# Kernel optimization log

Hardware: AMD Instinct MI355X
Metric: run time of the kernel (lower is better)

## Reference

```python
import jax, jax.numpy as jnp
import numpy as np

B, S, I, H = 32, 4096, 512, 512
NEG_INF = -1e18


def setup_inputs() -> dict:
    key = jax.random.key(0)
    ks = jax.random.split(key, 8)
    query = jax.random.normal(ks[0], (B, I), dtype=jnp.float32)
    kv = jax.random.normal(ks[1], (B, S, I), dtype=jnp.float32)
    mask = jax.random.randint(ks[2], (B, S), 0, 2).astype(jnp.bool_)
    # q_proj: Linear(I, H) with bias
    lim_q = 1.0 / np.sqrt(I)
    Wq = jax.random.uniform(ks[3], (H, I), minval=-lim_q, maxval=lim_q, dtype=jnp.float32)
    bq = jax.random.uniform(ks[4], (H,), minval=-lim_q, maxval=lim_q, dtype=jnp.float32)
    # k_proj: Conv1d(I, H, kernel_size=1) == pointwise linear; weight squeezed to [H, I]
    Wk = jax.random.uniform(ks[5], (H, I), minval=-lim_q, maxval=lim_q, dtype=jnp.float32)
    bk = jax.random.uniform(ks[6], (H,), minval=-lim_q, maxval=lim_q, dtype=jnp.float32)
    # out: Linear(H, 1, bias=False), init uniform(-1, 1); squeeze to [H]
    Wout = jax.random.uniform(ks[7], (H,), minval=-1.0, maxval=1.0, dtype=jnp.float32)
    return {"query": query, "key": kv, "mask": mask,
            "Wq": Wq, "bq": bq, "Wk": Wk, "bk": bk, "Wout": Wout}


def reference(query, key, mask, Wq, bq, Wk, bk, Wout):
    # q: [B, H]
    q = query @ Wq.T + bq
    # k: conv1d kernel-size-1 == per-position linear -> [B, S, H]
    k = jnp.einsum('bsi,hi->bsh', key, Wk) + bk
    # additive attention score: out((q + k)) -> [B, S]
    scores = jnp.einsum('bsh,h->bs', q[:, None, :] + k, Wout)
    attn_weight = jnp.where(mask, jnp.float32(NEG_INF), scores)
    attn_prob = jax.nn.softmax(attn_weight, axis=-1)
    # bmm(k^T-form [B, H, S], prob [B, S, 1]) -> [B, H]
    attn = jnp.einsum('bsh,bs->bh', k, attn_prob)
    return attn, attn_weight
```

## Files before the change

### kernel.cpp

```cpp
#include <hip/hip_runtime.h>
#include <math.h>

constexpr int B = 32, S = 4096, I = 512, H = 512;
constexpr int CH = 128;
constexpr int NCH = S / CH;
constexpr float NEGV = -1e18f;

constexpr size_t WS_WKD   = 0;
constexpr size_t WS_WQD   = 512;
constexpr size_t WS_CC    = 1024;
constexpr size_t WS_WKT   = 2048;
constexpr size_t WS_PARTS = WS_WKT + (size_t)I*H;

__global__ __launch_bounds__(256) void prep_kernel(
    const float* __restrict__ Wq, const float* __restrict__ bq,
    const float* __restrict__ Wk, const float* __restrict__ bk,
    const float* __restrict__ Wout, float* __restrict__ ws) {
  __shared__ float sh[64 * 65];
  int blk = blockIdx.x;
  int t = threadIdx.x, wv = t >> 6, ln = t & 63;

  if (blk < 16) {
    bool isQ = blk >= 8;
    const float* W = isQ ? Wq : Wk;
    float* out = ws + (isQ ? WS_WQD : WS_WKD);
    int j = (blk & 7) * 64;
    float p = 0.f;
    int h0 = wv * 128;
    #pragma unroll 4
    for (int h = h0; h < h0 + 128; ++h)
      p = fmaf(W[(size_t)h * I + j + ln], Wout[h], p);
    sh[wv * 64 + ln] = p;
    __syncthreads();
    if (t < 64) out[j + t] = sh[t] + sh[64 + t] + sh[128 + t] + sh[192 + t];
  } else if (blk == 16) {
    float p = 0.f;
    for (int h = t; h < H; h += 256) p = fmaf(bq[h] + bk[h], Wout[h], p);
    sh[t] = p;
    __syncthreads();
    for (int o = 128; o; o >>= 1) {
      if (t < o) sh[t] += sh[t + o];
      __syncthreads();
    }
    if (t == 0) ws[WS_CC] = sh[0];
  } else {
    int tt = blk - 17;
    int tr = tt >> 3, tc = tt & 7;
    float* wkT = ws + WS_WKT;
    #pragma unroll 4
    for (int k = 0; k < 16; ++k) {
      int r = wv * 16 + k;
      sh[r * 65 + ln] = Wk[(size_t)(tr * 64 + r) * I + tc * 64 + ln];
    }
    __syncthreads();
    #pragma unroll 4
    for (int k = 0; k < 16; ++k) {
      int r2 = wv * 16 + k;
      wkT[(size_t)(tc * 64 + r2) * H + tr * 64 + ln] = sh[ln * 65 + r2];
    }
  }
}

__global__ __launch_bounds__(256, 4) void main_kernel(
    const float* __restrict__ query,
    const float* __restrict__ key, const int* __restrict__ mask,
    float* __restrict__ ws, float* __restrict__ attn_w) {
  const float* wkd = ws + WS_WKD;
  const float* wqd = ws + WS_WQD;
  float* parts = ws + WS_PARTS;

  int b = blockIdx.x, cidx = blockIdx.y;
  int t = threadIdx.x, wv = t >> 6, ln = t & 63;

  float offb;
  {
    const float* qb = query + (size_t)b * I;
    float p = qb[ln] * wqd[ln];
    #pragma unroll
    for (int k = 1; k < 8; ++k)
      p = fmaf(qb[ln + 64 * k], wqd[ln + 64 * k], p);
    #pragma unroll
    for (int o = 32; o; o >>= 1) p += __shfl_xor(p, o, 64);
    offb = p + ws[WS_CC];
  }

  const float* kb = key + ((size_t)b * S + (size_t)cidx * CH) * I;
  const int* mrow = mask + (size_t)b * S + cidx * CH;
  float* awrow = attn_w + (size_t)b * S + cidx * CH;

  float4 wA = *(const float4*)(wkd + ln * 4);
  float4 wB = *(const float4*)(wkd + 256 + ln * 4);

  float m = -INFINITY, l = 0.f;
  float4 cA = {0.f, 0.f, 0.f, 0.f}, cB = {0.f, 0.f, 0.f, 0.f};

  constexpr int NIT = CH / 8;
  const float* lanep = kb + (size_t)(wv * 2) * I + ln * 4;
  constexpr int ROWSTEP = 8 * I;

  float4 uA0 = *(const float4*)(lanep);
  float4 uB0 = *(const float4*)(lanep + 256);
  float4 uA1 = *(const float4*)(lanep + 512);
  float4 uB1 = *(const float4*)(lanep + 768);
  float4 vA0 = *(const float4*)(lanep + ROWSTEP);
  float4 vB0 = *(const float4*)(lanep + ROWSTEP + 256);
  float4 vA1 = *(const float4*)(lanep + ROWSTEP + 512);
  float4 vB1 = *(const float4*)(lanep + ROWSTEP + 768);

  #pragma unroll 2
  for (int it = 0; it < NIT; ++it) {
    int s = wv * 2 + it * 8;
    int itn = (it + 2 < NIT) ? it + 2 : it;
    const float* kn = lanep + (size_t)itn * ROWSTEP;
    float4 nA0 = *(const float4*)(kn);
    float4 nB0 = *(const float4*)(kn + 256);
    float4 nA1 = *(const float4*)(kn + 512);
    float4 nB1 = *(const float4*)(kn + 768);

    float d0 = uA0.x * wA.x, d1 = uA1.x * wA.x;
    d0 = fmaf(uA0.y, wA.y, d0); d1 = fmaf(uA1.y, wA.y, d1);
    d0 = fmaf(uA0.z, wA.z, d0); d1 = fmaf(uA1.z, wA.z, d1);
    d0 = fmaf(uA0.w, wA.w, d0); d1 = fmaf(uA1.w, wA.w, d1);
    d0 = fmaf(uB0.x, wB.x, d0); d1 = fmaf(uB1.x, wB.x, d1);
    d0 = fmaf(uB0.y, wB.y, d0); d1 = fmaf(uB1.y, wB.y, d1);
    d0 = fmaf(uB0.z, wB.z, d0); d1 = fmaf(uB1.z, wB.z, d1);
    d0 = fmaf(uB0.w, wB.w, d0); d1 = fmaf(uB1.w, wB.w, d1);
    #pragma unroll
    for (int o = 32; o; o >>= 1) {
      d0 += __shfl_xor(d0, o, 64);
      d1 += __shfl_xor(d1, o, 64);
    }

    int2 mm = *(const int2*)(mrow + s);
    float s0 = mm.x ? NEGV : (offb + d0);
    float s1 = mm.y ? NEGV : (offb + d1);
    if (ln == 0) *(float2*)(awrow + s) = float2{s0, s1};

    float mx = fmaxf(s0, s1);
    if (mx > m) {
      float sc = __expf(m - mx);
      l *= sc;
      cA.x *= sc; cA.y *= sc; cA.z *= sc; cA.w *= sc;
      cB.x *= sc; cB.y *= sc; cB.z *= sc; cB.w *= sc;
      m = mx;
    }
    float e0 = __expf(s0 - m);
    float e1 = __expf(s1 - m);
    l += e0 + e1;
    cA.x = fmaf(e0, uA0.x, fmaf(e1, uA1.x, cA.x));
    cA.y = fmaf(e0, uA0.y, fmaf(e1, uA1.y, cA.y));
    cA.z = fmaf(e0, uA0.z, fmaf(e1, uA1.z, cA.z));
    cA.w = fmaf(e0, uA0.w, fmaf(e1, uA1.w, cA.w));
    cB.x = fmaf(e0, uB0.x, fmaf(e1, uB1.x, cB.x));
    cB.y = fmaf(e0, uB0.y, fmaf(e1, uB1.y, cB.y));
    cB.z = fmaf(e0, uB0.z, fmaf(e1, uB1.z, cB.z));
    cB.w = fmaf(e0, uB0.w, fmaf(e1, uB1.w, cB.w));

    uA0 = vA0; uB0 = vB0; uA1 = vA1; uB1 = vB1;
    vA0 = nA0; vB0 = nB0; vA1 = nA1; vB1 = nB1;
  }

  __shared__ float shm[4], shl[4];
  __shared__ float shc[4][512];
  if (ln == 0) { shm[wv] = m; shl[wv] = l; }
  *(float4*)&shc[wv][ln * 4] = cA;
  *(float4*)&shc[wv][256 + ln * 4] = cB;
  __syncthreads();

  float mb = fmaxf(fmaxf(shm[0], shm[1]), fmaxf(shm[2], shm[3]));
  float ew0 = __expf(shm[0] - mb), ew1 = __expf(shm[1] - mb);
  float ew2 = __expf(shm[2] - mb), ew3 = __expf(shm[3] - mb);
  float* slot = parts + ((size_t)b * NCH + cidx) * 514;
  if (t == 0) {
    slot[0] = mb;
    slot[1] = shl[0] * ew0 + shl[1] * ew1 + shl[2] * ew2 + shl[3] * ew3;
  }
  for (int i = t; i < I; i += 256) {
    float acc = shc[0][i] * ew0;
    acc = fmaf(shc[1][i], ew1, acc);
    acc = fmaf(shc[2][i], ew2, acc);
    acc = fmaf(shc[3][i], ew3, acc);
    slot[2 + i] = acc;
  }
}

__global__ __launch_bounds__(256) void finish_kernel(
    const float* __restrict__ bk, float* __restrict__ ws,
    float* __restrict__ attn) {
  const float* parts = ws + WS_PARTS;
  const float* wkT = ws + WS_WKT;
  int b = blockIdx.x, hq = blockIdx.y, t = threadIdx.x;

  __shared__ float eld[NCH], ctx[I], red[256];
  const float* pb = parts + (size_t)b * NCH * 514;

  float m = -INFINITY;
  #pragma unroll 8
  for (int p = 0; p < NCH; ++p) m = fmaxf(m, pb[p * 514]);
  float l = 0.f;
  #pragma unroll 8
  for (int p = 0; p < NCH; ++p) l = fmaf(pb[p * 514 + 1], __expf(pb[p * 514] - m), l);
  float invl = 1.f / l;
  if (t < NCH) eld[t] = __expf(pb[t * 514] - m) * invl;
  __syncthreads();

  {
    float a0 = 0.f, a1 = 0.f;
    #pragma unroll 8
    for (int p = 0; p < NCH; ++p) {
      float e = eld[p];
      a0 = fmaf(pb[p * 514 + 2 + t], e, a0);
      a1 = fmaf(pb[p * 514 + 258 + t], e, a1);
    }
    ctx[t] = a0;
    ctx[t + 256] = a1;
  }
  __syncthreads();

  int h = hq * 128 + (t & 127);
  int ih = t >> 7;
  const float* wc = wkT + (size_t)(ih * 256) * H + h;
  const float* cc = ctx + ih * 256;
  float acc = 0.f;
  #pragma unroll 16
  for (int i = 0; i < 256; ++i) acc = fmaf(cc[i], wc[(size_t)i * H], acc);
  red[t] = acc;
  __syncthreads();
  if (t < 128) attn[(size_t)b * H + h] = red[t] + red[t + 128] + bk[h];
}

extern "C" void kernel_launch(void* const* d_in, const int* in_sizes, int n_in,
                              void* d_out, int out_size, void* d_ws, size_t ws_size,
                              hipStream_t stream) {
  const float* query = (const float*)d_in[0];
  const float* key   = (const float*)d_in[1];
  const int*   mask  = (const int*)d_in[2];
  const float* Wq    = (const float*)d_in[3];
  const float* bq    = (const float*)d_in[4];
  const float* Wk    = (const float*)d_in[5];
  const float* bk    = (const float*)d_in[6];
  const float* Wout  = (const float*)d_in[7];

  float* attn   = (float*)d_out;
  float* attn_w = (float*)d_out + (size_t)B * H;
  float* ws     = (float*)d_ws;

  prep_kernel<<<81, 256, 0, stream>>>(Wq, bq, Wk, bk, Wout, ws);
  main_kernel<<<dim3(B, NCH), 256, 0, stream>>>(query, key, mask, ws, attn_w);
  finish_kernel<<<dim3(B, 4), 256, 0, stream>>>(bk, ws, attn);
}
```

Baseline: 81.71 us.

## Split weight-fold prep, precompute per-batch offset, drop Wk transpose in finish

The prep stage is split into two kernels. prepA spreads the Wout-folding of Wq/Wk over 128 blocks as partial sums, and a single-block prepB reduces those partials and computes each batch's query offset once, instead of every main_kernel block recomputing it. The Wk transpose into workspace is removed; finish_kernel now reads Wk rows directly with float4 loads, one thread per output h. This trades a fourth kernel launch and a serial single-block stage for less prep work and less redundant compute in main_kernel. The finish kernel's per-thread row reads are strided across threads, so the Wk access pattern changes.

```diff
diff --git a/kernel.cpp b/kernel.cpp
--- a/kernel.cpp
+++ b/kernel.cpp
@@ -7,82 +7,94 @@
 constexpr float NEGV = -1e18f;
 
 constexpr size_t WS_WKD   = 0;
-constexpr size_t WS_WQD   = 512;
-constexpr size_t WS_CC    = 1024;
-constexpr size_t WS_WKT   = 2048;
-constexpr size_t WS_PARTS = WS_WKT + (size_t)I*H;
-
-__global__ __launch_bounds__(256) void prep_kernel(
-    const float* __restrict__ Wq, const float* __restrict__ bq,
-    const float* __restrict__ Wk, const float* __restrict__ bk,
+constexpr size_t WS_OFF   = 512;
+constexpr size_t WS_PARTW = 1024;
+constexpr size_t WS_PARTS = 16384;
+
+__global__ __launch_bounds__(256) void prepA_kernel(
+    const float* __restrict__ Wq, const float* __restrict__ Wk,
     const float* __restrict__ Wout, float* __restrict__ ws) {
-  __shared__ float sh[64 * 65];
+  __shared__ float red[4][64];
   int blk = blockIdx.x;
   int t = threadIdx.x, wv = t >> 6, ln = t & 63;
-
-  if (blk < 16) {
-    bool isQ = blk >= 8;
-    const float* W = isQ ? Wq : Wk;
-    float* out = ws + (isQ ? WS_WQD : WS_WKD);
-    int j = (blk & 7) * 64;
-    float p = 0.f;
-    int h0 = wv * 128;
-    #pragma unroll 4
-    for (int h = h0; h < h0 + 128; ++h)
-      p = fmaf(W[(size_t)h * I + j + ln], Wout[h], p);
-    sh[wv * 64 + ln] = p;
+  bool isQ = blk >= 64;
+  const float* W = isQ ? Wq : Wk;
+  int sub = blk & 63;
+  int hs = sub >> 3, jt = sub & 7;
+  int j = jt * 64 + ln;
+
+  float acc = 0.f;
+  int h0 = hs * 64 + wv * 16;
+  #pragma unroll 4
+  for (int r = 0; r < 16; ++r) {
+    int h = h0 + r;
+    acc = fmaf(W[(size_t)h * I + j], Wout[h], acc);
+  }
+  red[wv][ln] = acc;
+  __syncthreads();
+  if (t < 64) {
+    float s = red[0][t] + red[1][t] + red[2][t] + red[3][t];
+    ws[WS_PARTW + (isQ ? 4096 : 0) + hs * 512 + jt * 64 + t] = s;
+  }
+}
+
+__global__ __launch_bounds__(256) void prepB_kernel(
+    const float* __restrict__ query, const float* __restrict__ bq,
+    const float* __restrict__ bk, const float* __restrict__ Wout,
+    float* __restrict__ ws) {
+  __shared__ float wq[512];
+  __shared__ float red2[256];
+  int t = threadIdx.x, wv = t >> 6, ln = t & 63;
+  const float* pk = ws + WS_PARTW;
+
+  #pragma unroll
+  for (int half = 0; half < 2; ++half) {
+    int c = t + half * 256;
+    float sk = 0.f, sq = 0.f;
+    #pragma unroll
+    for (int hs = 0; hs < 8; ++hs) {
+      sk += pk[hs * 512 + c];
+      sq += pk[4096 + hs * 512 + c];
+    }
+    ws[WS_WKD + c] = sk;
+    wq[c] = sq;
+  }
+
+  float p = 0.f;
+  p = fmaf(bq[t] + bk[t], Wout[t], p);
+  p = fmaf(bq[t + 256] + bk[t + 256], Wout[t + 256], p);
+  red2[t] = p;
+  __syncthreads();
+  for (int o = 128; o; o >>= 1) {
+    if (t < o) red2[t] += red2[t + o];
     __syncthreads();
-    if (t < 64) out[j + t] = sh[t] + sh[64 + t] + sh[128 + t] + sh[192 + t];
-  } else if (blk == 16) {
-    float p = 0.f;
-    for (int h = t; h < H; h += 256) p = fmaf(bq[h] + bk[h], Wout[h], p);
-    sh[t] = p;
-    __syncthreads();
-    for (int o = 128; o; o >>= 1) {
-      if (t < o) sh[t] += sh[t + o];
-      __syncthreads();
-    }
-    if (t == 0) ws[WS_CC] = sh[0];
-  } else {
-    int tt = blk - 17;
-    int tr = tt >> 3, tc = tt & 7;
-    float* wkT = ws + WS_WKT;
-    #pragma unroll 4
-    for (int k = 0; k < 16; ++k) {
-      int r = wv * 16 + k;
-      sh[r * 65 + ln] = Wk[(size_t)(tr * 64 + r) * I + tc * 64 + ln];
-    }
-    __syncthreads();
-    #pragma unroll 4
-    for (int k = 0; k < 16; ++k) {
-      int r2 = wv * 16 + k;
-      wkT[(size_t)(tc * 64 + r2) * H + tr * 64 + ln] = sh[ln * 65 + r2];
-    }
+  }
+  float ccv = red2[0];
+  __syncthreads();
+
+  for (int pass = 0; pass < 8; ++pass) {
+    int b = pass * 4 + wv;
+    const float* qb = query + (size_t)b * I;
+    float d = qb[ln] * wq[ln];
+    #pragma unroll
+    for (int k = 1; k < 8; ++k)
+      d = fmaf(qb[ln + 64 * k], wq[ln + 64 * k], d);
+    #pragma unroll
+    for (int o = 32; o; o >>= 1) d += __shfl_xor(d, o, 64);
+    if (ln == 0) ws[WS_OFF + b] = d + ccv;
   }
 }
 
 __global__ __launch_bounds__(256, 4) void main_kernel(
-    const float* __restrict__ query,
     const float* __restrict__ key, const int* __restrict__ mask,
     float* __restrict__ ws, float* __restrict__ attn_w) {
   const float* wkd = ws + WS_WKD;
-  const float* wqd = ws + WS_WQD;
   float* parts = ws + WS_PARTS;
 
   int b = blockIdx.x, cidx = blockIdx.y;
   int t = threadIdx.x, wv = t >> 6, ln = t & 63;
 
-  float offb;
-  {
-    const float* qb = query + (size_t)b * I;
-    float p = qb[ln] * wqd[ln];
-    #pragma unroll
-    for (int k = 1; k < 8; ++k)
-      p = fmaf(qb[ln + 64 * k], wqd[ln + 64 * k], p);
-    #pragma unroll
-    for (int o = 32; o; o >>= 1) p += __shfl_xor(p, o, 64);
-    offb = p + ws[WS_CC];
-  }
+  float offb = ws[WS_OFF + b];
 
   const float* kb = key + ((size_t)b * S + (size_t)cidx * CH) * I;
   const int* mrow = mask + (size_t)b * S + cidx * CH;
@@ -185,13 +197,12 @@
 }
 
 __global__ __launch_bounds__(256) void finish_kernel(
-    const float* __restrict__ bk, float* __restrict__ ws,
-    float* __restrict__ attn) {
+    const float* __restrict__ Wk, const float* __restrict__ bk,
+    float* __restrict__ ws, float* __restrict__ attn) {
   const float* parts = ws + WS_PARTS;
-  const float* wkT = ws + WS_WKT;
   int b = blockIdx.x, hq = blockIdx.y, t = threadIdx.x;
 
-  __shared__ float eld[NCH], ctx[I], red[256];
+  __shared__ float eld[NCH], ctx[I];
   const float* pb = parts + (size_t)b * NCH * 514;
 
   float m = -INFINITY;
@@ -217,16 +228,21 @@
   }
   __syncthreads();
 
-  int h = hq * 128 + (t & 127);
-  int ih = t >> 7;
-  const float* wc = wkT + (size_t)(ih * 256) * H + h;
-  const float* cc = ctx + ih * 256;
-  float acc = 0.f;
-  #pragma unroll 16
-  for (int i = 0; i < 256; ++i) acc = fmaf(cc[i], wc[(size_t)i * H], acc);
-  red[t] = acc;
-  __syncthreads();
-  if (t < 128) attn[(size_t)b * H + h] = red[t] + red[t + 128] + bk[h];
+  int h = hq * 256 + t;
+  const float4* wrow = (const float4*)(Wk + (size_t)h * I);
+  float a0 = 0.f, a1 = 0.f, a2 = 0.f, a3 = 0.f;
+  #pragma unroll 8
+  for (int c = 0; c < 128; c += 4) {
+    float4 w0 = wrow[c],     x0 = *(const float4*)(ctx + c * 4);
+    float4 w1 = wrow[c + 1], x1 = *(const float4*)(ctx + c * 4 + 4);
+    float4 w2 = wrow[c + 2], x2 = *(const float4*)(ctx + c * 4 + 8);
+    float4 w3 = wrow[c + 3], x3 = *(const float4*)(ctx + c * 4 + 12);
+    a0 = fmaf(w0.x, x0.x, fmaf(w0.y, x0.y, fmaf(w0.z, x0.z, fmaf(w0.w, x0.w, a0))));
+    a1 = fmaf(w1.x, x1.x, fmaf(w1.y, x1.y, fmaf(w1.z, x1.z, fmaf(w1.w, x1.w, a1))));
+    a2 = fmaf(w2.x, x2.x, fmaf(w2.y, x2.y, fmaf(w2.z, x2.z, fmaf(w2.w, x2.w, a2))));
+    a3 = fmaf(w3.x, x3.x, fmaf(w3.y, x3.y, fmaf(w3.z, x3.z, fmaf(w3.w, x3.w, a3))));
+  }
+  attn[(size_t)b * H + h] = (a0 + a1) + (a2 + a3) + bk[h];
 }
 
 extern "C" void kernel_launch(void* const* d_in, const int* in_sizes, int n_in,
@@ -245,7 +261,8 @@
   float* attn_w = (float*)d_out + (size_t)B * H;
   float* ws     = (float*)d_ws;
 
-  prep_kernel<<<81, 256, 0, stream>>>(Wq, bq, Wk, bk, Wout, ws);
-  main_kernel<<<dim3(B, NCH), 256, 0, stream>>>(query, key, mask, ws, attn_w);
-  finish_kernel<<<dim3(B, 4), 256, 0, stream>>>(bk, ws, attn);
-}
+  prepA_kernel<<<128, 256, 0, stream>>>(Wq, Wk, Wout, ws);
+  prepB_kernel<<<1, 256, 0, stream>>>(query, bq, bk, Wout, ws);
+  main_kernel<<<dim3(B, NCH), 256, 0, stream>>>(key, mask, ws, attn_w);
+  finish_kernel<<<dim3(B, 2), 256, 0, stream>>>(Wk, bk, ws, attn);
+}
```

Measured after the change: 85.37 us. 1.04x slower.
